# Kernel tuning notes

Measured on AMD Instinct MI355X. Metric: run time of the kernel, lower is better.

## Reference

```python
import jax, jax.numpy as jnp
import numpy as np

N_NODES = 100000
N_EDGES = 3200000
IN_CH, HID, OUT_CH = 128, 16, 64


def gcn_conv(x, W, b, row, col, n_nodes):
    # PyG GCNConv: add self loops, symmetric deg^{-1/2} normalization,
    # linear transform, scatter-add aggregation at target nodes (col).
    x = x @ W  # [N, out]
    deg = jax.ops.segment_sum(jnp.ones_like(col, dtype=x.dtype), col,
                              num_segments=n_nodes)  # includes self loops
    inv_sqrt = jnp.where(deg > 0, jax.lax.rsqrt(deg), 0.0)
    norm = inv_sqrt[row] * inv_sqrt[col]  # [E+N]
    msgs = x[row] * norm[:, None]  # gather + scale
    out = jax.ops.segment_sum(msgs, col, num_segments=n_nodes)
    return out + b


def setup_inputs() -> dict:
    key = jax.random.key(0)
    ks = jax.random.split(key, 12)
    x = jax.random.normal(ks[0], (N_NODES, IN_CH), dtype=jnp.float32)
    edge_index = jax.random.randint(ks[1], (2, N_EDGES), 0, N_NODES, dtype=jnp.int64)

    def glorot(k, fan_in, fan_out):
        s = jnp.sqrt(6.0 / (fan_in + fan_out))
        return jax.random.uniform(k, (fan_in, fan_out), jnp.float32, -s, s)

    return {
        'x': x,
        'edge_index': edge_index,
        'conv1_W': glorot(ks[2], IN_CH, HID),
        'conv1_b': jnp.zeros((HID,), jnp.float32),
        'conv2_W': glorot(ks[3], HID, OUT_CH),
        'conv2_b': jnp.zeros((OUT_CH,), jnp.float32),
        't1_W': glorot(ks[4], IN_CH, HID),
        't1_b': jnp.zeros((HID,), jnp.float32),
        't2_W': glorot(ks[5], HID, OUT_CH),
        't2_b': jnp.zeros((OUT_CH,), jnp.float32),
    }


def reference(x, edge_index, conv1_W, conv1_b, conv2_W, conv2_b,
              t1_W, t1_b, t2_W, t2_b):
    n = x.shape[0]
    # add self loops once (fixed shape)
    loops = jnp.arange(n, dtype=edge_index.dtype)
    row = jnp.concatenate([edge_index[0], loops])
    col = jnp.concatenate([edge_index[1], loops])

    identity1 = x @ t1_W + t1_b
    h = jax.nn.relu(gcn_conv(x, conv1_W, conv1_b, row, col, n)) + identity1
    identity2 = h @ t2_W + t2_b
    out = jax.nn.relu(gcn_conv(h, conv2_W, conv2_b, row, col, n)) + identity2
    return out
```

## Files before the change

### kernel.cpp

```cpp
#include <hip/hip_runtime.h>

#define INCH 128
#define C1   16
#define C2   64
#define LOCB 7
#define BNODES (1 << LOCB)
#define CAP  8192
#define ROWBITS 17
#define ROWMASK ((1 << ROWBITS) - 1)
#define SENT 0xFFFFFFFFu
#define ACC2P 9
#define FXS   16384.0f
#define INVFX 6.103515625e-05f
#define FXBH  524288.5f
#define BSH   19
#define BKT_T 1024
#define AGG_T 512

typedef int iv4 __attribute__((ext_vector_type(4)));
typedef unsigned short usv8 __attribute__((ext_vector_type(8)));

__device__ __forceinline__ unsigned short f2bf(float f) {
    unsigned u = __float_as_uint(f);
    return (unsigned short)((u + 0x7FFF + ((u >> 16) & 1)) >> 16);
}
__device__ __forceinline__ float bf2f(unsigned short s) {
    return __uint_as_float((unsigned)s << 16);
}

__global__ void binit_kernel(int* __restrict__ gcur, int K) {
    int t = blockIdx.x * blockDim.x + threadIdx.x;
    if (t < K) gcur[t] = t * CAP;
}

__global__ __launch_bounds__(BKT_T) void bucket_kernel(
    const int* __restrict__ row, const int* __restrict__ col,
    int* __restrict__ gcur, int* __restrict__ barr,
    int e, int n, int K, int nblocks)
{
    __shared__ int cnt[1024];
    __shared__ int cur[1024];
    __shared__ int sst[1024];
    int tid = threadIdx.x;
    int e4 = e >> 2;
    long b0 = (long)blockIdx.x * e4 / nblocks;
    long b1 = (long)(blockIdx.x + 1) * e4 / nblocks;
    const iv4* c4p = (const iv4*)col;
    const iv4* r4p = (const iv4*)row;
    cnt[tid] = 0;
    __syncthreads();
    for (long i = b0 + tid; i < b1; i += BKT_T) {
        iv4 c4 = c4p[i], r4 = r4p[i];
        #pragma unroll
        for (int k = 0; k < 4; ++k) {
            unsigned c = (unsigned)c4[k], r = (unsigned)r4[k];
            if (c < (unsigned)n && r < (unsigned)n)
                atomicAdd(&cnt[c >> LOCB], 1);
        }
    }
    if (blockIdx.x == 0) {
        for (int i = e4 * 4 + tid; i < e; i += BKT_T) {
            unsigned c = (unsigned)col[i], r = (unsigned)row[i];
            if (c < (unsigned)n && r < (unsigned)n)
                atomicAdd(&cnt[c >> LOCB], 1);
        }
    }
    __syncthreads();
    if (tid < K) {
        int c = cnt[tid];
        int start = c ? atomicAdd(&gcur[tid], (c + 15) & ~15) : 0;
        cur[tid] = start;
        sst[tid] = start;
    }
    __syncthreads();
    for (long i = b0 + tid; i < b1; i += BKT_T) {
        iv4 c4 = c4p[i], r4 = r4p[i];
        #pragma unroll
        for (int k = 0; k < 4; ++k) {
            unsigned c = (unsigned)c4[k], r = (unsigned)r4[k];
            if (c < (unsigned)n && r < (unsigned)n) {
                int b = c >> LOCB;
                int slot = atomicAdd(&cur[b], 1);
                if ((unsigned)slot < (unsigned)((b + 1) * CAP))
                    barr[slot] = (int)(r | ((c & (BNODES - 1)) << ROWBITS));
            }
        }
    }
    if (blockIdx.x == 0) {
        for (int i = e4 * 4 + tid; i < e; i += BKT_T) {
            unsigned c = (unsigned)col[i], r = (unsigned)row[i];
            if (c < (unsigned)n && r < (unsigned)n) {
                int b = c >> LOCB;
                int slot = atomicAdd(&cur[b], 1);
                if ((unsigned)slot < (unsigned)((b + 1) * CAP))
                    barr[slot] = (int)(r | ((c & (BNODES - 1)) << ROWBITS));
            }
        }
    }
    __syncthreads();
    if (tid < K) {
        int c = cnt[tid];
        if (c) {
            int start = sst[tid];
            int end = start + c;
            int re  = start + ((c + 15) & ~15);
            int lim = (tid + 1) * CAP;
            if (end > lim) end = lim;
            if (re  > lim) re  = lim;
            for (int j = end; j < re; ++j) barr[j] = (int)SENT;
        }
    }
}

__global__ __launch_bounds__(AGG_T) void degree_kernel(
    const int* __restrict__ barr, const int* __restrict__ gcur,
    float* __restrict__ inv, int* __restrict__ deg, int n)
{
    __shared__ int lcnt[BNODES];
    int b = blockIdx.x, tid = threadIdx.x;
    if (tid < BNODES) lcnt[tid] = 0;
    __syncthreads();
    int base = b * CAP;
    int len = gcur[b] - base;
    if (len < 0) len = 0;
    if (len > CAP) len = CAP;
    int len4 = len >> 2;
    const iv4* b4 = (const iv4*)(barr + base);
    for (int i = tid; i < len4; i += AGG_T) {
        iv4 p4 = b4[i];
        #pragma unroll
        for (int k = 0; k < 4; ++k) {
            unsigned pk = (unsigned)p4[k];
            if ((pk & ROWMASK) < (unsigned)n)
                atomicAdd(&lcnt[(pk >> ROWBITS) & (BNODES - 1)], 1);
        }
    }
    __syncthreads();
    if (tid < BNODES) {
        int node = (b << LOCB) + tid;
        if (node < n) {
            deg[node] = lcnt[tid];
            inv[node] = rsqrtf((float)lcnt[tid] + 1.0f);
        }
    }
}

__global__ __launch_bounds__(256) void linear1_kernel(
    const float* __restrict__ x, const float* __restrict__ W1,
    const float* __restrict__ T1, const float* __restrict__ t1b,
    const float* __restrict__ inv,
    unsigned short* __restrict__ xW1s_bf, float* __restrict__ xT1, int n)
{
    __shared__ float Wc[INCH][32];
    __shared__ float xs[16][INCH + 4];
    int tid = threadIdx.x;

    for (int i = tid; i < INCH * C1; i += 256) {
        int k = i / C1, c = i % C1;
        Wc[k][c]      = W1[i];
        Wc[k][c + 16] = T1[i];
    }
    int node0 = blockIdx.x * 16;
    for (int i = tid; i < 16 * (INCH / 4); i += 256) {
        int r = i / (INCH / 4);
        int cc = i % (INCH / 4);
        int node = node0 + r;
        float4 v = make_float4(0.f, 0.f, 0.f, 0.f);
        if (node < n) v = ((const float4*)x)[(size_t)node * (INCH / 4) + cc];
        ((float4*)&xs[r][0])[cc] = v;
    }
    __syncthreads();

    int ch = tid & 15, nl = tid >> 4;
    int node = node0 + nl;
    if (node >= n) return;
    float a1 = 0.f, a2 = 0.f;
    #pragma unroll
    for (int k = 0; k < INCH; ++k) {
        float xv = xs[nl][k];
        a1 += xv * Wc[k][ch];
        a2 += xv * Wc[k][ch + 16];
    }
    xW1s_bf[(node << 4) + ch] = f2bf(a1 * inv[node] * FXS);
    xT1[(node << 4) + ch]     = a2 + t1b[ch];
}

#define EDGE_ADDI64(PK, V)                                                    \
    do {                                                                      \
        if (((PK) & ROWMASK) < un) {                                          \
            unsigned long long* _a = &acc[(((PK) >> ROWBITS) & (BNODES - 1))][tb]; \
            _Pragma("unroll")                                                 \
            for (int _j = 0; _j < 4; ++_j) {                                  \
                unsigned _lo = (unsigned)(bf2f((V)[2 * _j])     + FXBH);      \
                unsigned _hi = (unsigned)(bf2f((V)[2 * _j + 1]) + FXBH);      \
                atomicAdd(&_a[_j], ((unsigned long long)_hi << 32) | _lo);    \
            }                                                                 \
        }                                                                     \
    } while (0)

#define GATHER_SCATTER(SRCBUF)                                                \
    {                                                                         \
        int jj = tid >> 1;                                                    \
        for (int i0 = jj * 4; i0 + 3 < len; i0 += (AGG_T * 2)) {              \
            iv4 w = *(const iv4*)(bp + i0);                                   \
            unsigned s0 = (unsigned)w[0] & ROWMASK, s1 = (unsigned)w[1] & ROWMASK; \
            unsigned s2 = (unsigned)w[2] & ROWMASK, s3 = (unsigned)w[3] & ROWMASK; \
            unsigned c0 = s0 < un ? s0 : 0u, c1 = s1 < un ? s1 : 0u;          \
            unsigned c2 = s2 < un ? s2 : 0u, c3 = s3 < un ? s3 : 0u;          \
            usv8 v0 = *(const usv8*)(SRCBUF + ((size_t)c0 << 4) + chb);       \
            usv8 v1 = *(const usv8*)(SRCBUF + ((size_t)c1 << 4) + chb);       \
            usv8 v2 = *(const usv8*)(SRCBUF + ((size_t)c2 << 4) + chb);       \
            usv8 v3 = *(const usv8*)(SRCBUF + ((size_t)c3 << 4) + chb);       \
            EDGE_ADDI64((unsigned)w[0], v0);                                  \
            EDGE_ADDI64((unsigned)w[1], v1);                                  \
            EDGE_ADDI64((unsigned)w[2], v2);                                  \
            EDGE_ADDI64((unsigned)w[3], v3);                                  \
        }                                                                     \
    }

__global__ __launch_bounds__(AGG_T) void agg1_bucket_kernel(
    const int* __restrict__ barr, const int* __restrict__ gcur,
    const float* __restrict__ inv, const int* __restrict__ deg,
    const unsigned short* __restrict__ xW1s_bf,
    const float* __restrict__ xT1, const float* __restrict__ b1,
    float* __restrict__ h, unsigned short* __restrict__ hs_bf, int n)
{
    __shared__ unsigned long long acc[BNODES][ACC2P];
    int b = blockIdx.x, tid = threadIdx.x;
    for (int i = tid; i < BNODES * ACC2P; i += AGG_T) (&acc[0][0])[i] = 0ull;
    __syncthreads();

    int base = b * CAP;
    int len = gcur[b] - base;
    if (len < 0) len = 0;
    if (len > CAP) len = CAP;
    const int* bp = barr + base;
    unsigned un = (unsigned)n;
    int chb = (tid & 1) << 3;
    int tb  = (tid & 1) << 2;

    GATHER_SCATTER(xW1s_bf)
    __syncthreads();

    for (int t = tid; t < BNODES * C1; t += AGG_T) {
        int loc = t >> 4, ch = t & 15;
        int node = (b << LOCB) + loc;
        if (node >= n) continue;
        int idx = (node << 4) + ch;
        unsigned long long w = acc[loc][ch >> 1];
        unsigned wd = (ch & 1) ? (unsigned)(w >> 32) : (unsigned)w;
        int sv = (int)(wd - ((unsigned)deg[node] << BSH));
        float ic = inv[node];
        float v = ((float)sv + bf2f(xW1s_bf[idx])) * INVFX * ic + b1[ch];
        float hv = fmaxf(v, 0.f) + xT1[idx];
        h[idx]     = hv;
        hs_bf[idx] = f2bf(hv * ic * FXS);
    }
}

__global__ __launch_bounds__(AGG_T) void agg2_bucket_kernel(
    const int* __restrict__ barr, const int* __restrict__ gcur,
    const float* __restrict__ inv, const int* __restrict__ deg,
    const unsigned short* __restrict__ hs_bf, const float* __restrict__ h,
    const float* __restrict__ W2, const float* __restrict__ T2,
    const float* __restrict__ b2, const float* __restrict__ t2b,
    float* __restrict__ out, int n)
{
    __shared__ unsigned long long acc[BNODES][ACC2P];
    __shared__ float Wc[C1][128];
    __shared__ float h_s[BNODES][C1];
    __shared__ float accf[BNODES][C1 + 1];
    int b = blockIdx.x, tid = threadIdx.x;
    for (int i = tid; i < BNODES * ACC2P; i += AGG_T) (&acc[0][0])[i] = 0ull;
    for (int i = tid; i < C1 * 128; i += AGG_T) {
        int k = i >> 7, c = i & 127;
        Wc[k][c] = (c < 64) ? W2[k * C2 + c] : T2[k * C2 + (c - 64)];
    }
    {
        int node0 = b << LOCB;
        for (int t = tid; t < BNODES * C1 / 4; t += AGG_T) {
            float4 v = make_float4(0.f, 0.f, 0.f, 0.f);
            if (node0 + (t >> 2) < n) v = ((const float4*)h)[(size_t)node0 * 4 + t];
            ((float4*)&h_s[0][0])[t] = v;
        }
    }
    __syncthreads();

    int base = b * CAP;
    int len = gcur[b] - base;
    if (len < 0) len = 0;
    if (len > CAP) len = CAP;
    const int* bp = barr + base;
    unsigned un = (unsigned)n;
    int chb = (tid & 1) << 3;
    int tb  = (tid & 1) << 2;

    GATHER_SCATTER(hs_bf)
    __syncthreads();

    for (int t = tid; t < BNODES * C1; t += AGG_T) {
        int loc = t >> 4, ch = t & 15;
        int node = (b << LOCB) + loc;
        float v = 0.f;
        if (node < n) {
            unsigned long long w = acc[loc][ch >> 1];
            unsigned wd = (ch & 1) ? (unsigned)(w >> 32) : (unsigned)w;
            int sv = (int)(wd - ((unsigned)deg[node] << BSH));
            v = ((float)sv + bf2f(hs_bf[(node << 4) + ch])) * INVFX * inv[node];
        }
        accf[loc][ch] = v;
    }
    __syncthreads();

    int och = tid & 63, g = tid >> 6;
    float w1r[C1], w2r[C1];
    #pragma unroll
    for (int k = 0; k < C1; ++k) { w1r[k] = Wc[k][och]; w2r[k] = Wc[k][och + 64]; }
    float bb = b2[och], tb2 = t2b[och];
    for (int q = 0; q < 16; ++q) {
        int loc = (g << 4) + q;
        int node2 = (b << LOCB) + loc;
        if (node2 >= n) continue;
        float s1 = bb, s2 = tb2;
        #pragma unroll
        for (int k = 0; k < C1; ++k) {
            s1 += accf[loc][k] * w1r[k];
            s2 += h_s[loc][k]  * w2r[k];
        }
        out[(size_t)node2 * C2 + och] = fmaxf(s1, 0.f) + s2;
    }
}

extern "C" void kernel_launch(void* const* d_in, const int* in_sizes, int n_in,
                              void* d_out, int out_size, void* d_ws, size_t ws_size,
                              hipStream_t stream) {
    const float* x   = (const float*)d_in[0];
    const int*   ei  = (const int*)d_in[1];
    const float* W1  = (const float*)d_in[2];
    const float* b1  = (const float*)d_in[3];
    const float* W2  = (const float*)d_in[4];
    const float* b2  = (const float*)d_in[5];
    const float* T1  = (const float*)d_in[6];
    const float* t1b = (const float*)d_in[7];
    const float* T2  = (const float*)d_in[8];
    const float* t2b = (const float*)d_in[9];
    float* out = (float*)d_out;

    const int n = in_sizes[0] / INCH;
    const int e = in_sizes[1] / 2;
    const int* row = ei;
    const int* col = ei + e;
    const int K = (n + BNODES - 1) >> LOCB;

    char* ws = (char*)d_ws;
    int*   gcur  = (int*)ws;                          ws += 4096;
    float* inv   = (float*)ws;                        ws += (size_t)n * 4;
    int*   deg   = (int*)ws;                          ws += (size_t)n * 4;
    float* xT1   = (float*)ws;                        ws += (size_t)n * C1 * 4;
    float* h     = (float*)ws;                        ws += (size_t)n * C1 * 4;
    unsigned short* xW1s_bf = (unsigned short*)ws;    ws += (size_t)n * C1 * 2;
    unsigned short* hs_bf   = (unsigned short*)ws;    ws += (size_t)n * C1 * 2;
    int*   barr  = (int*)ws;                          ws += (size_t)K * CAP * 4;

    const int nbb = 390;

    binit_kernel  <<<(K + 255) / 256, 256, 0, stream>>>(gcur, K);
    bucket_kernel <<<nbb, BKT_T, 0, stream>>>(row, col, gcur, barr, e, n, K, nbb);
    degree_kernel <<<K, AGG_T, 0, stream>>>(barr, gcur, inv, deg, n);

    linear1_kernel <<<(n + 15) / 16, 256, 0, stream>>>(x, W1, T1, t1b, inv, xW1s_bf, xT1, n);
    agg1_bucket_kernel<<<K, AGG_T, 0, stream>>>(barr, gcur, inv, deg, xW1s_bf, xT1, b1, h, hs_bf, n);
    agg2_bucket_kernel<<<K, AGG_T, 0, stream>>>(barr, gcur, inv, deg, hs_bf, h,
                                                W2, T2, b2, t2b, out, n);
}
```

Measured before the change: 249.6 us.

## Fold degree count into bucketing and gather pre-biased fixed-point features

```diff
diff --git a/kernel.cpp b/kernel.cpp
--- a/kernel.cpp
+++ b/kernel.cpp
@@ -18,24 +18,18 @@
 #define AGG_T 512
 
 typedef int iv4 __attribute__((ext_vector_type(4)));
-typedef unsigned short usv8 __attribute__((ext_vector_type(8)));
-
-__device__ __forceinline__ unsigned short f2bf(float f) {
-    unsigned u = __float_as_uint(f);
-    return (unsigned short)((u + 0x7FFF + ((u >> 16) & 1)) >> 16);
-}
-__device__ __forceinline__ float bf2f(unsigned short s) {
-    return __uint_as_float((unsigned)s << 16);
-}
-
-__global__ void binit_kernel(int* __restrict__ gcur, int K) {
+typedef unsigned long long ulv2 __attribute__((ext_vector_type(2)));
+
+__global__ void binit_kernel(int* __restrict__ gcur, int K,
+                             int* __restrict__ deg, int n) {
     int t = blockIdx.x * blockDim.x + threadIdx.x;
     if (t < K) gcur[t] = t * CAP;
+    if (t < n) deg[t] = 0;
 }
 
 __global__ __launch_bounds__(BKT_T) void bucket_kernel(
     const int* __restrict__ row, const int* __restrict__ col,
-    int* __restrict__ gcur, int* __restrict__ barr,
+    int* __restrict__ gcur, int* __restrict__ barr, int* __restrict__ deg,
     int e, int n, int K, int nblocks)
 {
     __shared__ int cnt[1024];
@@ -54,15 +48,19 @@
         #pragma unroll
         for (int k = 0; k < 4; ++k) {
             unsigned c = (unsigned)c4[k], r = (unsigned)r4[k];
-            if (c < (unsigned)n && r < (unsigned)n)
+            if (c < (unsigned)n && r < (unsigned)n) {
                 atomicAdd(&cnt[c >> LOCB], 1);
+                atomicAdd(&deg[c], 1);
+            }
         }
     }
     if (blockIdx.x == 0) {
         for (int i = e4 * 4 + tid; i < e; i += BKT_T) {
             unsigned c = (unsigned)col[i], r = (unsigned)row[i];
-            if (c < (unsigned)n && r < (unsigned)n)
+            if (c < (unsigned)n && r < (unsigned)n) {
                 atomicAdd(&cnt[c >> LOCB], 1);
+                atomicAdd(&deg[c], 1);
+            }
         }
     }
     __syncthreads();
@@ -112,44 +110,11 @@
     }
 }
 
-__global__ __launch_bounds__(AGG_T) void degree_kernel(
-    const int* __restrict__ barr, const int* __restrict__ gcur,
-    float* __restrict__ inv, int* __restrict__ deg, int n)
-{
-    __shared__ int lcnt[BNODES];
-    int b = blockIdx.x, tid = threadIdx.x;
-    if (tid < BNODES) lcnt[tid] = 0;
-    __syncthreads();
-    int base = b * CAP;
-    int len = gcur[b] - base;
-    if (len < 0) len = 0;
-    if (len > CAP) len = CAP;
-    int len4 = len >> 2;
-    const iv4* b4 = (const iv4*)(barr + base);
-    for (int i = tid; i < len4; i += AGG_T) {
-        iv4 p4 = b4[i];
-        #pragma unroll
-        for (int k = 0; k < 4; ++k) {
-            unsigned pk = (unsigned)p4[k];
-            if ((pk & ROWMASK) < (unsigned)n)
-                atomicAdd(&lcnt[(pk >> ROWBITS) & (BNODES - 1)], 1);
-        }
-    }
-    __syncthreads();
-    if (tid < BNODES) {
-        int node = (b << LOCB) + tid;
-        if (node < n) {
-            deg[node] = lcnt[tid];
-            inv[node] = rsqrtf((float)lcnt[tid] + 1.0f);
-        }
-    }
-}
-
 __global__ __launch_bounds__(256) void linear1_kernel(
     const float* __restrict__ x, const float* __restrict__ W1,
     const float* __restrict__ T1, const float* __restrict__ t1b,
-    const float* __restrict__ inv,
-    unsigned short* __restrict__ xW1s_bf, float* __restrict__ xT1, int n)
+    const int* __restrict__ deg,
+    unsigned* __restrict__ xW1u, float* __restrict__ xT1, int n)
 {
     __shared__ float Wc[INCH][32];
     __shared__ float xs[16][INCH + 4];
@@ -181,20 +146,19 @@
         a1 += xv * Wc[k][ch];
         a2 += xv * Wc[k][ch + 16];
     }
-    xW1s_bf[(node << 4) + ch] = f2bf(a1 * inv[node] * FXS);
-    xT1[(node << 4) + ch]     = a2 + t1b[ch];
-}
-
-#define EDGE_ADDI64(PK, V)                                                    \
+    float ic = rsqrtf((float)(deg[node] + 1));
+    xW1u[(node << 4) + ch] = (unsigned)(a1 * ic * FXS + FXBH);
+    xT1[(node << 4) + ch]  = a2 + t1b[ch];
+}
+
+#define EDGE_GS(PK, GA, GB)                                                   \
     do {                                                                      \
         if (((PK) & ROWMASK) < un) {                                          \
             unsigned long long* _a = &acc[(((PK) >> ROWBITS) & (BNODES - 1))][tb]; \
-            _Pragma("unroll")                                                 \
-            for (int _j = 0; _j < 4; ++_j) {                                  \
-                unsigned _lo = (unsigned)(bf2f((V)[2 * _j])     + FXBH);      \
-                unsigned _hi = (unsigned)(bf2f((V)[2 * _j + 1]) + FXBH);      \
-                atomicAdd(&_a[_j], ((unsigned long long)_hi << 32) | _lo);    \
-            }                                                                 \
+            atomicAdd(&_a[0], (GA)[0]);                                       \
+            atomicAdd(&_a[1], (GA)[1]);                                       \
+            atomicAdd(&_a[2], (GB)[0]);                                       \
+            atomicAdd(&_a[3], (GB)[1]);                                       \
         }                                                                     \
     } while (0)
 
@@ -207,23 +171,26 @@
             unsigned s2 = (unsigned)w[2] & ROWMASK, s3 = (unsigned)w[3] & ROWMASK; \
             unsigned c0 = s0 < un ? s0 : 0u, c1 = s1 < un ? s1 : 0u;          \
             unsigned c2 = s2 < un ? s2 : 0u, c3 = s3 < un ? s3 : 0u;          \
-            usv8 v0 = *(const usv8*)(SRCBUF + ((size_t)c0 << 4) + chb);       \
-            usv8 v1 = *(const usv8*)(SRCBUF + ((size_t)c1 << 4) + chb);       \
-            usv8 v2 = *(const usv8*)(SRCBUF + ((size_t)c2 << 4) + chb);       \
-            usv8 v3 = *(const usv8*)(SRCBUF + ((size_t)c3 << 4) + chb);       \
-            EDGE_ADDI64((unsigned)w[0], v0);                                  \
-            EDGE_ADDI64((unsigned)w[1], v1);                                  \
-            EDGE_ADDI64((unsigned)w[2], v2);                                  \
-            EDGE_ADDI64((unsigned)w[3], v3);                                  \
+            const ulv2* p0 = (const ulv2*)(SRCBUF + ((size_t)c0 << 4) + chb); \
+            const ulv2* p1 = (const ulv2*)(SRCBUF + ((size_t)c1 << 4) + chb); \
+            const ulv2* p2 = (const ulv2*)(SRCBUF + ((size_t)c2 << 4) + chb); \
+            const ulv2* p3 = (const ulv2*)(SRCBUF + ((size_t)c3 << 4) + chb); \
+            ulv2 ga0 = p0[0], gb0 = p0[1];                                    \
+            ulv2 ga1 = p1[0], gb1 = p1[1];                                    \
+            ulv2 ga2 = p2[0], gb2 = p2[1];                                    \
+            ulv2 ga3 = p3[0], gb3 = p3[1];                                    \
+            EDGE_GS((unsigned)w[0], ga0, gb0);                                \
+            EDGE_GS((unsigned)w[1], ga1, gb1);                                \
+            EDGE_GS((unsigned)w[2], ga2, gb2);                                \
+            EDGE_GS((unsigned)w[3], ga3, gb3);                                \
         }                                                                     \
     }
 
 __global__ __launch_bounds__(AGG_T) void agg1_bucket_kernel(
     const int* __restrict__ barr, const int* __restrict__ gcur,
-    const float* __restrict__ inv, const int* __restrict__ deg,
-    const unsigned short* __restrict__ xW1s_bf,
+    const int* __restrict__ deg, const unsigned* __restrict__ xW1u,
     const float* __restrict__ xT1, const float* __restrict__ b1,
-    float* __restrict__ h, unsigned short* __restrict__ hs_bf, int n)
+    float* __restrict__ h, unsigned* __restrict__ hu, int n)
 {
     __shared__ unsigned long long acc[BNODES][ACC2P];
     int b = blockIdx.x, tid = threadIdx.x;
@@ -239,29 +206,30 @@
     int chb = (tid & 1) << 3;
     int tb  = (tid & 1) << 2;
 
-    GATHER_SCATTER(xW1s_bf)
-    __syncthreads();
-
+    GATHER_SCATTER(xW1u)
+    __syncthreads();
+
+    const unsigned* au = (const unsigned*)&acc[0][0];
     for (int t = tid; t < BNODES * C1; t += AGG_T) {
         int loc = t >> 4, ch = t & 15;
         int node = (b << LOCB) + loc;
         if (node >= n) continue;
         int idx = (node << 4) + ch;
-        unsigned long long w = acc[loc][ch >> 1];
-        unsigned wd = (ch & 1) ? (unsigned)(w >> 32) : (unsigned)w;
-        int sv = (int)(wd - ((unsigned)deg[node] << BSH));
-        float ic = inv[node];
-        float v = ((float)sv + bf2f(xW1s_bf[idx])) * INVFX * ic + b1[ch];
+        int dg = deg[node];
+        unsigned wd = au[loc * (2 * ACC2P) + ch];
+        int tot = (int)(wd + xW1u[idx] - ((unsigned)(dg + 1) << BSH));
+        float ic = rsqrtf((float)(dg + 1));
+        float v = (float)tot * INVFX * ic + b1[ch];
         float hv = fmaxf(v, 0.f) + xT1[idx];
-        h[idx]     = hv;
-        hs_bf[idx] = f2bf(hv * ic * FXS);
+        h[idx]  = hv;
+        hu[idx] = (unsigned)(hv * ic * FXS + FXBH);
     }
 }
 
 __global__ __launch_bounds__(AGG_T) void agg2_bucket_kernel(
     const int* __restrict__ barr, const int* __restrict__ gcur,
-    const float* __restrict__ inv, const int* __restrict__ deg,
-    const unsigned short* __restrict__ hs_bf, const float* __restrict__ h,
+    const int* __restrict__ deg, const unsigned* __restrict__ hu,
+    const float* __restrict__ h,
     const float* __restrict__ W2, const float* __restrict__ T2,
     const float* __restrict__ b2, const float* __restrict__ t2b,
     float* __restrict__ out, int n)
@@ -295,18 +263,19 @@
     int chb = (tid & 1) << 3;
     int tb  = (tid & 1) << 2;
 
-    GATHER_SCATTER(hs_bf)
-    __syncthreads();
-
+    GATHER_SCATTER(hu)
+    __syncthreads();
+
+    const unsigned* au = (const unsigned*)&acc[0][0];
     for (int t = tid; t < BNODES * C1; t += AGG_T) {
         int loc = t >> 4, ch = t & 15;
         int node = (b << LOCB) + loc;
         float v = 0.f;
         if (node < n) {
-            unsigned long long w = acc[loc][ch >> 1];
-            unsigned wd = (ch & 1) ? (unsigned)(w >> 32) : (unsigned)w;
-            int sv = (int)(wd - ((unsigned)deg[node] << BSH));
-            v = ((float)sv + bf2f(hs_bf[(node << 4) + ch])) * INVFX * inv[node];
+            int dg = deg[node];
+            unsigned wd = au[loc * (2 * ACC2P) + ch];
+            int tot = (int)(wd + hu[(node << 4) + ch] - ((unsigned)(dg + 1) << BSH));
+            v = (float)tot * INVFX * rsqrtf((float)(dg + 1));
         }
         accf[loc][ch] = v;
     }
@@ -353,23 +322,21 @@
     const int K = (n + BNODES - 1) >> LOCB;
 
     char* ws = (char*)d_ws;
-    int*   gcur  = (int*)ws;                          ws += 4096;
-    float* inv   = (float*)ws;                        ws += (size_t)n * 4;
-    int*   deg   = (int*)ws;                          ws += (size_t)n * 4;
-    float* xT1   = (float*)ws;                        ws += (size_t)n * C1 * 4;
-    float* h     = (float*)ws;                        ws += (size_t)n * C1 * 4;
-    unsigned short* xW1s_bf = (unsigned short*)ws;    ws += (size_t)n * C1 * 2;
-    unsigned short* hs_bf   = (unsigned short*)ws;    ws += (size_t)n * C1 * 2;
-    int*   barr  = (int*)ws;                          ws += (size_t)K * CAP * 4;
+    int*      gcur = (int*)ws;                        ws += 4096;
+    int*      deg  = (int*)ws;                        ws += (size_t)n * 4;
+    float*    xT1  = (float*)ws;                      ws += (size_t)n * C1 * 4;
+    float*    h    = (float*)ws;                      ws += (size_t)n * C1 * 4;
+    unsigned* xW1u = (unsigned*)ws;                   ws += (size_t)n * C1 * 4;
+    unsigned* hu   = (unsigned*)ws;                   ws += (size_t)n * C1 * 4;
+    int*      barr = (int*)ws;                        ws += (size_t)K * CAP * 4;
 
     const int nbb = 390;
 
-    binit_kernel  <<<(K + 255) / 256, 256, 0, stream>>>(gcur, K);
-    bucket_kernel <<<nbb, BKT_T, 0, stream>>>(row, col, gcur, barr, e, n, K, nbb);
-    degree_kernel <<<K, AGG_T, 0, stream>>>(barr, gcur, inv, deg, n);
-
-    linear1_kernel <<<(n + 15) / 16, 256, 0, stream>>>(x, W1, T1, t1b, inv, xW1s_bf, xT1, n);
-    agg1_bucket_kernel<<<K, AGG_T, 0, stream>>>(barr, gcur, inv, deg, xW1s_bf, xT1, b1, h, hs_bf, n);
-    agg2_bucket_kernel<<<K, AGG_T, 0, stream>>>(barr, gcur, inv, deg, hs_bf, h,
+    binit_kernel  <<<(n + 255) / 256, 256, 0, stream>>>(gcur, K, deg, n);
+    bucket_kernel <<<nbb, BKT_T, 0, stream>>>(row, col, gcur, barr, deg, e, n, K, nbb);
+
+    linear1_kernel <<<(n + 15) / 16, 256, 0, stream>>>(x, W1, T1, t1b, deg, xW1u, xT1, n);
+    agg1_bucket_kernel<<<K, AGG_T, 0, stream>>>(barr, gcur, deg, xW1u, xT1, b1, h, hu, n);
+    agg2_bucket_kernel<<<K, AGG_T, 0, stream>>>(barr, gcur, deg, hu, h,
                                                 W2, T2, b2, t2b, out, n);
 }
```

New measurement: 372.8 us. 1.49x slower.
